# Optimization experiments

Measured on AMD Instinct MI355X. Metric: run time of the kernel, lower is better.

Reference implementation:

```python
import jax, jax.numpy as jnp
import numpy as np

E = 16          # number of experts
K = 2           # top-k routing
D = 1024        # model dim
F = 512         # expert ffn dim
T = 4096        # tokens
C = 2048


def setup_inputs() -> dict:
    key = jax.random.key(0)
    k1, k2, k3, k4, k5, k6 = jax.random.split(key, 6)
    return {
        "hidden_states": jax.random.normal(k1, (T, D), jnp.float32),
        "topk_indices": jax.random.randint(k2, (T, K), 0, E, jnp.int64),
        "topk_weights": jax.random.uniform(k3, (T, K), jnp.float32),
        "w_gate": jax.random.normal(k4, (E, D, F), jnp.float32) * 0.02,
        "w_up": jax.random.normal(k5, (E, D, F), jnp.float32) * 0.02,
        "w_down": jax.random.normal(k6, (E, F, D), jnp.float32) * 0.02,
    }


def reference(hidden_states, topk_indices, topk_weights, w_gate, w_up, w_down):
    Tn, d = hidden_states.shape
    k = topk_indices.shape[1]
    TK = Tn * k

    # ---- dispatch_tokens: group (token, expert) pairs by expert id ----
    flat_e = topk_indices.reshape(-1)                 # [TK] expert id per slot
    flat_w = topk_weights.reshape(-1)                 # [TK]
    flat_t = jnp.arange(TK) // k                      # [TK] source token id
    order = jnp.argsort(flat_e)                       # sort slots by expert
    se, st, sw = flat_e[order], flat_t[order], flat_w[order]
    counts = jnp.bincount(flat_e, length=E)           # tokens per expert
    starts = jnp.cumsum(counts) - counts              # exclusive prefix sum
    pos = jnp.arange(TK) - starts[se]                 # position within expert bucket
    valid = pos < C
    slot = jnp.where(valid, se * C + pos, E * C)      # overflow -> scratch row

    # gather tokens into padded per-expert buffers [E, C, D]
    buf = jnp.zeros((E * C + 1, d), hidden_states.dtype).at[slot].set(hidden_states[st])
    xe = buf[: E * C].reshape(E, C, d)

    # ---- per-expert gated-SiLU MLP via grouped GEMMs ----
    h = jax.nn.silu(jnp.einsum('ecd,edf->ecf', xe, w_gate)) * jnp.einsum('ecd,edf->ecf', xe, w_up)
    ye = jnp.einsum('ecf,efd->ecd', h, w_down).reshape(E * C, d)

    # ---- weighted scatter-add combine (index_add_) ----
    contrib = ye[jnp.minimum(slot, E * C - 1)] * (sw * valid.astype(sw.dtype))[:, None]
    out = jnp.zeros((Tn, d), topk_weights.dtype).at[st].add(contrib)
    return out.astype(hidden_states.dtype)
```

## Files before the change

kernel.cpp:

```cpp
#include <hip/hip_runtime.h>
#include <hip/hip_bf16.h>

constexpr int E_ = 16, K_ = 2, D_ = 1024, F_ = 512, T_ = 4096;
constexpr int TK_ = T_ * K_;
constexpr int CAP_ = 2048;
constexpr int BM_ = 128;
constexpr int ROWS_MAX = 10240;

constexpr size_t SZ_W   = (size_t)E_ * F_ * D_ * 2;
constexpr size_t OFF_WDT  = 0;
constexpr size_t OFF_WGT  = OFF_WDT + SZ_W;
constexpr size_t OFF_WUT  = OFF_WGT + SZ_W;
constexpr size_t OFF_XG   = OFF_WUT + SZ_W;
constexpr size_t SZ_XG  = (size_t)ROWS_MAX * D_ * 2;
constexpr size_t OFF_H    = OFF_XG + SZ_XG;
constexpr size_t SZ_H   = (size_t)ROWS_MAX * F_ * 2;
constexpr size_t OFF_META = OFF_H + SZ_H;
constexpr size_t OFF_YE   = OFF_WGT;
static_assert(OFF_YE + (size_t)ROWS_MAX * D_ * 4 <= OFF_H, "Ye overlaps live buffers");

typedef __attribute__((ext_vector_type(8))) short short8;
typedef __attribute__((ext_vector_type(4))) float float4v;

__device__ __forceinline__ unsigned short f2bf(float f) {
  union { float f; unsigned int u; } v; v.f = f;
  unsigned int r = (v.u + 0x7fffu + ((v.u >> 16) & 1u)) >> 16;
  return (unsigned short)r;
}

__device__ __forceinline__ void load_lds16(const unsigned short* g, unsigned short* l) {
  __builtin_amdgcn_global_load_lds(
      (const __attribute__((address_space(1))) unsigned int*)g,
      (__attribute__((address_space(3))) unsigned int*)l,
      16, 0, 0);
}

__device__ __forceinline__ void barrier_nodrain() {
  asm volatile("" ::: "memory");
  __builtin_amdgcn_s_barrier();
  asm volatile("" ::: "memory");
}

__launch_bounds__(1024)
__global__ void dispatch_k(const int* __restrict__ idx, const float* __restrict__ tw,
                           int* __restrict__ cnt_c, int* __restrict__ off_al,
                           int* __restrict__ row_token, float* __restrict__ row_weight,
                           int* __restrict__ slot_row) {
  __shared__ int hist[E_], offs[E_], ctr[E_];
  int tid = threadIdx.x;
  if (tid < E_) hist[tid] = 0;
  __syncthreads();
  for (int i = tid; i < TK_; i += 1024) atomicAdd(&hist[idx[i]], 1);
  __syncthreads();
  if (tid == 0) {
    int run = 0;
    for (int e = 0; e < E_; ++e) {
      int c = hist[e] > CAP_ ? CAP_ : hist[e];
      cnt_c[e] = c; off_al[e] = run; offs[e] = run; ctr[e] = 0;
      run += (c + BM_ - 1) & ~(BM_ - 1);
    }
  }
  __syncthreads();
  for (int r = tid; r < ROWS_MAX; r += 1024) row_token[r] = -1;
  __syncthreads();
  for (int i = tid; i < TK_; i += 1024) {
    int e = idx[i];
    int r = atomicAdd(&ctr[e], 1);
    int row = -1;
    if (r < CAP_) {
      row = offs[e] + r;
      row_token[row] = i >> 1;
      row_weight[row] = tw[i];
    }
    slot_row[i] = row;
  }
}

__global__ void gather_k(const float* __restrict__ hidden, const int* __restrict__ row_token,
                         unsigned short* __restrict__ Xg) {
  int r = blockIdx.x;
  int tok = row_token[r];
  int c = threadIdx.x * 4;
  ushort4 o;
  if (tok >= 0) {
    float4 v = *(const float4*)(hidden + (size_t)tok * D_ + c);
    o.x = f2bf(v.x); o.y = f2bf(v.y); o.z = f2bf(v.z); o.w = f2bf(v.w);
  } else {
    o.x = 0; o.y = 0; o.z = 0; o.w = 0;
  }
  *(ushort4*)(Xg + (size_t)r * D_ + c) = o;
}

__launch_bounds__(256)
__global__ void transpose_all_k(const float* __restrict__ wg, const float* __restrict__ wu,
                                const float* __restrict__ wd,
                                unsigned short* __restrict__ WgT, unsigned short* __restrict__ WuT,
                                unsigned short* __restrict__ WdT) {
  __shared__ float tile[64][65];
  int z = blockIdx.y;
  int kind = z >> 4, e = z & 15;
  int R = (kind == 2) ? F_ : D_;
  int C = (kind == 2) ? D_ : F_;
  const float* s = ((kind == 0) ? wg : (kind == 1) ? wu : wd) + (size_t)e * R * C;
  unsigned short* d = ((kind == 0) ? WgT : (kind == 1) ? WuT : WdT) + (size_t)e * R * C;
  int tilesX = C >> 6;
  int t = blockIdx.x;
  int r0 = (t / tilesX) * 64, c0 = (t % tilesX) * 64;

  int lr = threadIdx.x >> 4;
  int lc = (threadIdx.x & 15) * 4;
#pragma unroll
  for (int it = 0; it < 4; ++it) {
    int row = lr + it * 16;
    float4 v = *(const float4*)(s + (size_t)(r0 + row) * C + (c0 + lc));
    tile[row][lc + 0] = v.x; tile[row][lc + 1] = v.y;
    tile[row][lc + 2] = v.z; tile[row][lc + 3] = v.w;
  }
  __syncthreads();

  int w = threadIdx.x >> 6, l = threadIdx.x & 63;
#pragma unroll
  for (int it = 0; it < 2; ++it) {
    int c = (it * 4 + w) * 8 + (l >> 3);
    int r8 = (l & 7) * 8;
    short8 o;
#pragma unroll
    for (int j = 0; j < 8; ++j) o[j] = (short)f2bf(tile[r8 + j][c]);
    *(short8*)(d + (size_t)(c0 + c) * R + (r0 + r8)) = o;
  }
}


__launch_bounds__(256)
__global__ void gemm1_k(const unsigned short* __restrict__ Xg,
                        const unsigned short* __restrict__ WgT,
                        const unsigned short* __restrict__ WuT,
                        unsigned short* __restrict__ Hbuf,
                        const int* __restrict__ cnt_c, const int* __restrict__ off_al) {
  int bid = blockIdx.x;
  int swz = (bid & 7) * 512 + (bid >> 3);
  int e = swz >> 8, mt = (swz >> 3) & 31, nt = swz & 7;
  int cnt = cnt_c[e];
  if (mt * 64 >= cnt) return;
  int rbase = off_al[e] + mt * 64;

  __shared__ unsigned short lA[2][64 * 64];
  __shared__ unsigned short lBg[2][64 * 64];
  __shared__ unsigned short lBu[2][64 * 64];

  int tid = threadIdx.x, wid = tid >> 6, lane = tid & 63;
  int wm = wid >> 1, wn = wid & 1;
  int quad = lane >> 4, l15 = lane & 15;
  int sw = l15 & 7;

  const unsigned short* gA = Xg + (size_t)rbase * D_;
  const unsigned short* gB0 = WgT + ((size_t)e * F_ + nt * 64) * D_;
  const unsigned short* gB1 = WuT + ((size_t)e * F_ + nt * 64) * D_;

  float4v accg[2][2], accu[2][2];
#pragma unroll
  for (int i = 0; i < 2; ++i)
#pragma unroll
    for (int j = 0; j < 2; ++j) {
      accg[i][j] = (float4v){0.f, 0.f, 0.f, 0.f};
      accu[i][j] = (float4v){0.f, 0.f, 0.f, 0.f};
    }

  auto stage = [&](int buf, int k0) {
#pragma unroll
    for (int it = 0; it < 2; ++it) {
      int fw = it * 256 + wid * 64;
      int f = fw + lane;
      int row = f >> 3, c8 = (f & 7) ^ (row & 7);
      size_t go = (size_t)row * D_ + k0 + c8 * 8;
      load_lds16(gA + go, &lA[buf][fw * 8]);
      load_lds16(gB0 + go, &lBg[buf][fw * 8]);
      load_lds16(gB1 + go, &lBu[buf][fw * 8]);
    }
  };

  stage(0, 0);

  for (int kt = 0; kt < 16; ++kt) {
    int cur = kt & 1;
    if (kt + 1 < 16) {
      stage(cur ^ 1, (kt + 1) * 64);
      asm volatile("s_waitcnt vmcnt(6)" ::: "memory");
    } else {
      asm volatile("s_waitcnt vmcnt(0)" ::: "memory");
    }
    __builtin_amdgcn_sched_barrier(0);
    barrier_nodrain();
#pragma unroll
    for (int kc = 0; kc < 2; ++kc) {
      short8 af[2], bg[2], bu[2];
#pragma unroll
      for (int i = 0; i < 2; ++i) {
        int r = wm * 32 + i * 16 + l15;
        af[i] = *(const short8*)&lA[cur][r * 64 + ((kc * 4 + quad) ^ sw) * 8];
      }
#pragma unroll
      for (int j = 0; j < 2; ++j) {
        int n = wn * 32 + j * 16 + l15;
        bg[j] = *(const short8*)&lBg[cur][n * 64 + ((kc * 4 + quad) ^ sw) * 8];
        bu[j] = *(const short8*)&lBu[cur][n * 64 + ((kc * 4 + quad) ^ sw) * 8];
      }
#pragma unroll
      for (int i = 0; i < 2; ++i)
#pragma unroll
        for (int j = 0; j < 2; ++j) {
          accg[i][j] = __builtin_amdgcn_mfma_f32_16x16x32_bf16(af[i], bg[j], accg[i][j], 0, 0, 0);
          accu[i][j] = __builtin_amdgcn_mfma_f32_16x16x32_bf16(af[i], bu[j], accu[i][j], 0, 0, 0);
        }
    }
    barrier_nodrain();
  }

  int rem = cnt - mt * 64;
#pragma unroll
  for (int i = 0; i < 2; ++i)
#pragma unroll
    for (int j = 0; j < 2; ++j)
#pragma unroll
      for (int r = 0; r < 4; ++r) {
        int row = wm * 32 + i * 16 + quad * 4 + r;
        if (row < rem) {
          float g = accg[i][j][r], u = accu[i][j][r];
          float h = (g / (1.f + __expf(-g))) * u;
          int n = nt * 64 + wn * 32 + j * 16 + l15;
          Hbuf[(size_t)(rbase + row) * F_ + n] = f2bf(h);
        }
      }
}

__launch_bounds__(256)
__global__ void gemm2_k(const unsigned short* __restrict__ Hbuf,
                        const unsigned short* __restrict__ WdT,
                        float* __restrict__ Ye,
                        const int* __restrict__ cnt_c, const int* __restrict__ off_al) {
  int bid = blockIdx.x;
  int swz = (bid & 7) * 512 + (bid >> 3);
  int e = swz >> 8, mt = (swz >> 3) & 31, nt = swz & 7;
  int cnt = cnt_c[e];
  if (mt * 64 >= cnt) return;
  int rbase = off_al[e] + mt * 64;

  __shared__ unsigned short lA[2][64 * 64];
  __shared__ unsigned short lB[2][128 * 64];

  int tid = threadIdx.x, wid = tid >> 6, lane = tid & 63;
  int wm = wid >> 1, wn = wid & 1;
  int quad = lane >> 4, l15 = lane & 15;
  int sw = l15 & 7;

  const unsigned short* gA = Hbuf + (size_t)rbase * F_;
  const unsigned short* gB = WdT + ((size_t)e * D_ + nt * 128) * F_;

  float4v acc[2][4];
#pragma unroll
  for (int i = 0; i < 2; ++i)
#pragma unroll
    for (int j = 0; j < 4; ++j) acc[i][j] = (float4v){0.f, 0.f, 0.f, 0.f};

  auto stage = [&](int buf, int k0) {
#pragma unroll
    for (int it = 0; it < 2; ++it) {
      int fw = it * 256 + wid * 64;
      int f = fw + lane;
      int row = f >> 3, c8 = (f & 7) ^ (row & 7);
      load_lds16(gA + (size_t)row * F_ + k0 + c8 * 8, &lA[buf][fw * 8]);
    }
#pragma unroll
    for (int it = 0; it < 4; ++it) {
      int fw = it * 256 + wid * 64;
      int f = fw + lane;
      int row = f >> 3, c8 = (f & 7) ^ (row & 7);
      load_lds16(gB + (size_t)row * F_ + k0 + c8 * 8, &lB[buf][fw * 8]);
    }
  };

  stage(0, 0);

  for (int kt = 0; kt < 8; ++kt) {
    int cur = kt & 1;
    if (kt + 1 < 8) {
      stage(cur ^ 1, (kt + 1) * 64);
      asm volatile("s_waitcnt vmcnt(6)" ::: "memory");
    } else {
      asm volatile("s_waitcnt vmcnt(0)" ::: "memory");
    }
    __builtin_amdgcn_sched_barrier(0);
    barrier_nodrain();
#pragma unroll
    for (int kc = 0; kc < 2; ++kc) {
      short8 af[2], bf[4];
#pragma unroll
      for (int i = 0; i < 2; ++i) {
        int r = wm * 32 + i * 16 + l15;
        af[i] = *(const short8*)&lA[cur][r * 64 + ((kc * 4 + quad) ^ sw) * 8];
      }
#pragma unroll
      for (int j = 0; j < 4; ++j) {
        int n = wn * 64 + j * 16 + l15;
        bf[j] = *(const short8*)&lB[cur][n * 64 + ((kc * 4 + quad) ^ sw) * 8];
      }
#pragma unroll
      for (int i = 0; i < 2; ++i)
#pragma unroll
        for (int j = 0; j < 4; ++j)
          acc[i][j] = __builtin_amdgcn_mfma_f32_16x16x32_bf16(af[i], bf[j], acc[i][j], 0, 0, 0);
    }
    barrier_nodrain();
  }

  int rem = cnt - mt * 64;
#pragma unroll
  for (int i = 0; i < 2; ++i)
#pragma unroll
    for (int r = 0; r < 4; ++r) {
      int row = wm * 32 + i * 16 + quad * 4 + r;
      if (row < rem) {
        float* yp = Ye + (size_t)(rbase + row) * D_ + nt * 128 + wn * 64 + l15;
#pragma unroll
        for (int j = 0; j < 4; ++j) yp[j * 16] = acc[i][j][r];
      }
    }
}

__global__ void combine_k(const float* __restrict__ Ye, const int* __restrict__ slot_row,
                          const float* __restrict__ row_weight, float* __restrict__ out) {
  int t = blockIdx.x;
  int c = threadIdx.x * 4;
  int r0 = slot_row[2 * t], r1 = slot_row[2 * t + 1];
  float4 acc = {0.f, 0.f, 0.f, 0.f};
  if (r0 >= 0) {
    float w = row_weight[r0];
    float4 y = *(const float4*)(Ye + (size_t)r0 * D_ + c);
    acc.x = w * y.x; acc.y = w * y.y; acc.z = w * y.z; acc.w = w * y.w;
  }
  if (r1 >= 0) {
    float w = row_weight[r1];
    float4 y = *(const float4*)(Ye + (size_t)r1 * D_ + c);
    acc.x += w * y.x; acc.y += w * y.y; acc.z += w * y.z; acc.w += w * y.w;
  }
  *(float4*)(out + (size_t)t * D_ + c) = acc;
}

extern "C" void kernel_launch(void* const* d_in, const int* in_sizes, int n_in,
                              void* d_out, int out_size, void* d_ws, size_t ws_size,
                              hipStream_t stream) {
  const float* hidden  = (const float*)d_in[0];
  const int*   topkidx = (const int*)d_in[1];
  const float* topkw   = (const float*)d_in[2];
  const float* w_gate  = (const float*)d_in[3];
  const float* w_up    = (const float*)d_in[4];
  const float* w_down  = (const float*)d_in[5];
  float* out = (float*)d_out;

  char* ws = (char*)d_ws;
  unsigned short* WdT = (unsigned short*)(ws + OFF_WDT);
  unsigned short* WgT = (unsigned short*)(ws + OFF_WGT);
  unsigned short* WuT = (unsigned short*)(ws + OFF_WUT);
  unsigned short* Xg  = (unsigned short*)(ws + OFF_XG);
  unsigned short* Hb  = (unsigned short*)(ws + OFF_H);
  float* Ye           = (float*)(ws + OFF_YE);
  int* meta           = (int*)(ws + OFF_META);
  int* cnt_c     = meta;
  int* off_al    = meta + 16;
  int* row_token = meta + 32;
  float* row_weight = (float*)(meta + 32 + ROWS_MAX);
  int* slot_row  = meta + 32 + 2 * ROWS_MAX;

  dispatch_k<<<1, 1024, 0, stream>>>(topkidx, topkw, cnt_c, off_al, row_token, row_weight,
                                     slot_row);
  transpose_all_k<<<dim3(128, 48), 256, 0, stream>>>(w_gate, w_up, w_down, WgT, WuT, WdT);
  gather_k<<<ROWS_MAX, 256, 0, stream>>>(hidden, row_token, Xg);

  gemm1_k<<<4096, 256, 0, stream>>>(Xg, WgT, WuT, Hb, cnt_c, off_al);
  gemm2_k<<<4096, 256, 0, stream>>>(Hb, WdT, Ye, cnt_c, off_al);
  combine_k<<<T_, 256, 0, stream>>>(Ye, slot_row, row_weight, out);
}
```

Before: 232.7 us.

## Fuse fp32 weight conversion into grouped GEMMs and parallelize dispatch per expert

Drops the separate transpose/convert kernel. The GEMMs now load fp32 weights straight from global memory into registers, convert them to bf16 with packed cvt instructions, and write them transposed into LDS, with the B tiles single-buffered. Dispatch is split into one block per expert, and the workspace layout shrinks because the transposed weight copies are gone. This removes a full pass over 96MB of fp32 weights, but every GEMM tile re-reads fp32 weights with strided scalar loads, so global traffic per tile roughly doubles and more time may be exposed on loads.

```diff
diff --git a/kernel.cpp b/kernel.cpp
--- a/kernel.cpp
+++ b/kernel.cpp
@@ -7,17 +7,12 @@
 constexpr int BM_ = 128;
 constexpr int ROWS_MAX = 10240;
 
-constexpr size_t SZ_W   = (size_t)E_ * F_ * D_ * 2;
-constexpr size_t OFF_WDT  = 0;
-constexpr size_t OFF_WGT  = OFF_WDT + SZ_W;
-constexpr size_t OFF_WUT  = OFF_WGT + SZ_W;
-constexpr size_t OFF_XG   = OFF_WUT + SZ_W;
-constexpr size_t SZ_XG  = (size_t)ROWS_MAX * D_ * 2;
-constexpr size_t OFF_H    = OFF_XG + SZ_XG;
-constexpr size_t SZ_H   = (size_t)ROWS_MAX * F_ * 2;
-constexpr size_t OFF_META = OFF_H + SZ_H;
-constexpr size_t OFF_YE   = OFF_WGT;
-static_assert(OFF_YE + (size_t)ROWS_MAX * D_ * 4 <= OFF_H, "Ye overlaps live buffers");
+constexpr size_t OFF_H    = 0;
+constexpr size_t SZ_H     = (size_t)ROWS_MAX * F_ * 2;
+constexpr size_t OFF_XG   = OFF_H + SZ_H;
+constexpr size_t OFF_YE   = OFF_XG;
+constexpr size_t SZ_YE    = (size_t)ROWS_MAX * D_ * 4;
+constexpr size_t OFF_META = OFF_XG + SZ_YE;
 
 typedef __attribute__((ext_vector_type(8))) short short8;
 typedef __attribute__((ext_vector_type(4))) float float4v;
@@ -26,6 +21,12 @@
   union { float f; unsigned int u; } v; v.f = f;
   unsigned int r = (v.u + 0x7fffu + ((v.u >> 16) & 1u)) >> 16;
   return (unsigned short)r;
+}
+
+__device__ __forceinline__ unsigned int cvt2(float lo, float hi) {
+  unsigned int r;
+  asm("v_cvt_pk_bf16_f32 %0, %1, %2" : "=v"(r) : "v"(lo), "v"(hi));
+  return r;
 }
 
 __device__ __forceinline__ void load_lds16(const unsigned short* g, unsigned short* l) {
@@ -41,38 +42,44 @@
   asm volatile("" ::: "memory");
 }
 
-__launch_bounds__(1024)
+__launch_bounds__(256)
 __global__ void dispatch_k(const int* __restrict__ idx, const float* __restrict__ tw,
                            int* __restrict__ cnt_c, int* __restrict__ off_al,
                            int* __restrict__ row_token, float* __restrict__ row_weight,
                            int* __restrict__ slot_row) {
-  __shared__ int hist[E_], offs[E_], ctr[E_];
-  int tid = threadIdx.x;
+  __shared__ int hist[E_];
+  __shared__ int off_s, pad_s, cnt_s;
+  int e = blockIdx.x, tid = threadIdx.x;
   if (tid < E_) hist[tid] = 0;
+  if (tid == 0) cnt_s = 0;
   __syncthreads();
-  for (int i = tid; i < TK_; i += 1024) atomicAdd(&hist[idx[i]], 1);
+  for (int i = tid; i < TK_; i += 256) atomicAdd(&hist[idx[i]], 1);
   __syncthreads();
   if (tid == 0) {
-    int run = 0;
-    for (int e = 0; e < E_; ++e) {
-      int c = hist[e] > CAP_ ? CAP_ : hist[e];
-      cnt_c[e] = c; off_al[e] = run; offs[e] = run; ctr[e] = 0;
+    int run = 0, off = 0, myc = 0;
+    for (int ee = 0; ee < E_; ++ee) {
+      int c = hist[ee] > CAP_ ? CAP_ : hist[ee];
+      if (ee == e) { off = run; myc = c; }
       run += (c + BM_ - 1) & ~(BM_ - 1);
     }
+    off_s = off; pad_s = (myc + BM_ - 1) & ~(BM_ - 1);
+    cnt_c[e] = myc; off_al[e] = off;
   }
   __syncthreads();
-  for (int r = tid; r < ROWS_MAX; r += 1024) row_token[r] = -1;
+  int off = off_s, pad = pad_s;
+  for (int r = tid; r < pad; r += 256) row_token[off + r] = -1;
   __syncthreads();
-  for (int i = tid; i < TK_; i += 1024) {
-    int e = idx[i];
-    int r = atomicAdd(&ctr[e], 1);
-    int row = -1;
-    if (r < CAP_) {
-      row = offs[e] + r;
-      row_token[row] = i >> 1;
-      row_weight[row] = tw[i];
-    }
-    slot_row[i] = row;
+  for (int i = tid; i < TK_; i += 256) {
+    if (idx[i] == e) {
+      int r = atomicAdd(&cnt_s, 1);
+      int row = -1;
+      if (r < CAP_) {
+        row = off + r;
+        row_token[row] = i >> 1;
+        row_weight[row] = tw[i];
+      }
+      slot_row[i] = row;
+    }
   }
 }
 
@@ -82,7 +89,7 @@
   int tok = row_token[r];
   int c = threadIdx.x * 4;
   ushort4 o;
-  if (tok >= 0) {
+  if ((unsigned)tok < (unsigned)T_) {
     float4 v = *(const float4*)(hidden + (size_t)tok * D_ + c);
     o.x = f2bf(v.x); o.y = f2bf(v.y); o.z = f2bf(v.z); o.w = f2bf(v.w);
   } else {
@@ -91,50 +98,10 @@
   *(ushort4*)(Xg + (size_t)r * D_ + c) = o;
 }
 
-__launch_bounds__(256)
-__global__ void transpose_all_k(const float* __restrict__ wg, const float* __restrict__ wu,
-                                const float* __restrict__ wd,
-                                unsigned short* __restrict__ WgT, unsigned short* __restrict__ WuT,
-                                unsigned short* __restrict__ WdT) {
-  __shared__ float tile[64][65];
-  int z = blockIdx.y;
-  int kind = z >> 4, e = z & 15;
-  int R = (kind == 2) ? F_ : D_;
-  int C = (kind == 2) ? D_ : F_;
-  const float* s = ((kind == 0) ? wg : (kind == 1) ? wu : wd) + (size_t)e * R * C;
-  unsigned short* d = ((kind == 0) ? WgT : (kind == 1) ? WuT : WdT) + (size_t)e * R * C;
-  int tilesX = C >> 6;
-  int t = blockIdx.x;
-  int r0 = (t / tilesX) * 64, c0 = (t % tilesX) * 64;
-
-  int lr = threadIdx.x >> 4;
-  int lc = (threadIdx.x & 15) * 4;
-#pragma unroll
-  for (int it = 0; it < 4; ++it) {
-    int row = lr + it * 16;
-    float4 v = *(const float4*)(s + (size_t)(r0 + row) * C + (c0 + lc));
-    tile[row][lc + 0] = v.x; tile[row][lc + 1] = v.y;
-    tile[row][lc + 2] = v.z; tile[row][lc + 3] = v.w;
-  }
-  __syncthreads();
-
-  int w = threadIdx.x >> 6, l = threadIdx.x & 63;
-#pragma unroll
-  for (int it = 0; it < 2; ++it) {
-    int c = (it * 4 + w) * 8 + (l >> 3);
-    int r8 = (l & 7) * 8;
-    short8 o;
-#pragma unroll
-    for (int j = 0; j < 8; ++j) o[j] = (short)f2bf(tile[r8 + j][c]);
-    *(short8*)(d + (size_t)(c0 + c) * R + (r0 + r8)) = o;
-  }
-}
-
-
-__launch_bounds__(256)
+
+__launch_bounds__(256, 4)
 __global__ void gemm1_k(const unsigned short* __restrict__ Xg,
-                        const unsigned short* __restrict__ WgT,
-                        const unsigned short* __restrict__ WuT,
+                        const float* __restrict__ Wg, const float* __restrict__ Wu,
                         unsigned short* __restrict__ Hbuf,
                         const int* __restrict__ cnt_c, const int* __restrict__ off_al) {
   int bid = blockIdx.x;
@@ -145,8 +112,8 @@
   int rbase = off_al[e] + mt * 64;
 
   __shared__ unsigned short lA[2][64 * 64];
-  __shared__ unsigned short lBg[2][64 * 64];
-  __shared__ unsigned short lBu[2][64 * 64];
+  __shared__ unsigned short lBg[64 * 64];
+  __shared__ unsigned short lBu[64 * 64];
 
   int tid = threadIdx.x, wid = tid >> 6, lane = tid & 63;
   int wm = wid >> 1, wn = wid & 1;
@@ -154,8 +121,8 @@
   int sw = l15 & 7;
 
   const unsigned short* gA = Xg + (size_t)rbase * D_;
-  const unsigned short* gB0 = WgT + ((size_t)e * F_ + nt * 64) * D_;
-  const unsigned short* gB1 = WuT + ((size_t)e * F_ + nt * 64) * D_;
+  const float* gW0 = Wg + (size_t)e * D_ * F_ + nt * 64 + lane;
+  const float* gW1 = Wu + (size_t)e * D_ * F_ + nt * 64 + lane;
 
   float4v accg[2][2], accu[2][2];
 #pragma unroll
@@ -166,29 +133,57 @@
       accu[i][j] = (float4v){0.f, 0.f, 0.f, 0.f};
     }
 
-  auto stage = [&](int buf, int k0) {
+  float bga[8], bgb[8], bua[8], bub[8];
+  auto loadB = [&](int k0) {
+#pragma unroll
+    for (int j = 0; j < 8; ++j) {
+      size_t ra = (size_t)(k0 + wid * 8 + j) * F_;
+      size_t rb = (size_t)(k0 + (wid + 4) * 8 + j) * F_;
+      bga[j] = gW0[ra]; bgb[j] = gW0[rb];
+      bua[j] = gW1[ra]; bub[j] = gW1[rb];
+    }
+  };
+  int sA = (wid ^ (lane & 7)) * 8, sB = ((wid + 4) ^ (lane & 7)) * 8;
+  int wb = lane * 64;
+  auto writeB = [&]() {
+    uint4 p;
+    p.x = cvt2(bga[0], bga[1]); p.y = cvt2(bga[2], bga[3]);
+    p.z = cvt2(bga[4], bga[5]); p.w = cvt2(bga[6], bga[7]);
+    *(uint4*)&lBg[wb + sA] = p;
+    p.x = cvt2(bgb[0], bgb[1]); p.y = cvt2(bgb[2], bgb[3]);
+    p.z = cvt2(bgb[4], bgb[5]); p.w = cvt2(bgb[6], bgb[7]);
+    *(uint4*)&lBg[wb + sB] = p;
+    p.x = cvt2(bua[0], bua[1]); p.y = cvt2(bua[2], bua[3]);
+    p.z = cvt2(bua[4], bua[5]); p.w = cvt2(bua[6], bua[7]);
+    *(uint4*)&lBu[wb + sA] = p;
+    p.x = cvt2(bub[0], bub[1]); p.y = cvt2(bub[2], bub[3]);
+    p.z = cvt2(bub[4], bub[5]); p.w = cvt2(bub[6], bub[7]);
+    *(uint4*)&lBu[wb + sB] = p;
+  };
+  auto stageA = [&](int buf, int k0) {
 #pragma unroll
     for (int it = 0; it < 2; ++it) {
       int fw = it * 256 + wid * 64;
       int f = fw + lane;
       int row = f >> 3, c8 = (f & 7) ^ (row & 7);
-      size_t go = (size_t)row * D_ + k0 + c8 * 8;
-      load_lds16(gA + go, &lA[buf][fw * 8]);
-      load_lds16(gB0 + go, &lBg[buf][fw * 8]);
-      load_lds16(gB1 + go, &lBu[buf][fw * 8]);
-    }
-  };
-
-  stage(0, 0);
+      load_lds16(gA + (size_t)row * D_ + k0 + c8 * 8, &lA[buf][fw * 8]);
+    }
+  };
+
+  loadB(0);
+  stageA(0, 0);
 
   for (int kt = 0; kt < 16; ++kt) {
     int cur = kt & 1;
+    writeB();
     if (kt + 1 < 16) {
-      stage(cur ^ 1, (kt + 1) * 64);
-      asm volatile("s_waitcnt vmcnt(6)" ::: "memory");
+      loadB((kt + 1) * 64);
+      stageA(cur ^ 1, (kt + 1) * 64);
+      asm volatile("s_waitcnt vmcnt(34)" ::: "memory");
     } else {
       asm volatile("s_waitcnt vmcnt(0)" ::: "memory");
     }
+    asm volatile("s_waitcnt lgkmcnt(0)" ::: "memory");
     __builtin_amdgcn_sched_barrier(0);
     barrier_nodrain();
 #pragma unroll
@@ -202,8 +197,8 @@
 #pragma unroll
       for (int j = 0; j < 2; ++j) {
         int n = wn * 32 + j * 16 + l15;
-        bg[j] = *(const short8*)&lBg[cur][n * 64 + ((kc * 4 + quad) ^ sw) * 8];
-        bu[j] = *(const short8*)&lBu[cur][n * 64 + ((kc * 4 + quad) ^ sw) * 8];
+        bg[j] = *(const short8*)&lBg[n * 64 + ((kc * 4 + quad) ^ sw) * 8];
+        bu[j] = *(const short8*)&lBu[n * 64 + ((kc * 4 + quad) ^ sw) * 8];
       }
 #pragma unroll
       for (int i = 0; i < 2; ++i)
@@ -233,9 +228,9 @@
       }
 }
 
-__launch_bounds__(256)
+__launch_bounds__(256, 4)
 __global__ void gemm2_k(const unsigned short* __restrict__ Hbuf,
-                        const unsigned short* __restrict__ WdT,
+                        const float* __restrict__ Wd,
                         float* __restrict__ Ye,
                         const int* __restrict__ cnt_c, const int* __restrict__ off_al) {
   int bid = blockIdx.x;
@@ -246,7 +241,7 @@
   int rbase = off_al[e] + mt * 64;
 
   __shared__ unsigned short lA[2][64 * 64];
-  __shared__ unsigned short lB[2][128 * 64];
+  __shared__ unsigned short lB[128 * 64];
 
   int tid = threadIdx.x, wid = tid >> 6, lane = tid & 63;
   int wm = wid >> 1, wn = wid & 1;
@@ -254,7 +249,7 @@
   int sw = l15 & 7;
 
   const unsigned short* gA = Hbuf + (size_t)rbase * F_;
-  const unsigned short* gB = WdT + ((size_t)e * D_ + nt * 128) * F_;
+  const float* gW = Wd + (size_t)e * F_ * D_ + nt * 128 + lane;
 
   float4v acc[2][4];
 #pragma unroll
@@ -262,7 +257,26 @@
 #pragma unroll
     for (int j = 0; j < 4; ++j) acc[i][j] = (float4v){0.f, 0.f, 0.f, 0.f};
 
-  auto stage = [&](int buf, int k0) {
+  float b[4][8];
+  auto loadB = [&](int k0) {
+#pragma unroll
+    for (int c = 0; c < 4; ++c)
+#pragma unroll
+      for (int j = 0; j < 8; ++j)
+        b[c][j] = gW[(size_t)(k0 + (wid + (c >> 1) * 4) * 8 + j) * D_ + (c & 1) * 64];
+  };
+  auto writeB = [&]() {
+#pragma unroll
+    for (int c = 0; c < 4; ++c) {
+      int n = (c & 1) * 64 + lane;
+      int s = ((wid + (c >> 1) * 4) ^ (lane & 7)) * 8;
+      uint4 p;
+      p.x = cvt2(b[c][0], b[c][1]); p.y = cvt2(b[c][2], b[c][3]);
+      p.z = cvt2(b[c][4], b[c][5]); p.w = cvt2(b[c][6], b[c][7]);
+      *(uint4*)&lB[n * 64 + s] = p;
+    }
+  };
+  auto stageA = [&](int buf, int k0) {
 #pragma unroll
     for (int it = 0; it < 2; ++it) {
       int fw = it * 256 + wid * 64;
@@ -270,25 +284,22 @@
       int row = f >> 3, c8 = (f & 7) ^ (row & 7);
       load_lds16(gA + (size_t)row * F_ + k0 + c8 * 8, &lA[buf][fw * 8]);
     }
-#pragma unroll
-    for (int it = 0; it < 4; ++it) {
-      int fw = it * 256 + wid * 64;
-      int f = fw + lane;
-      int row = f >> 3, c8 = (f & 7) ^ (row & 7);
-      load_lds16(gB + (size_t)row * F_ + k0 + c8 * 8, &lB[buf][fw * 8]);
-    }
-  };
-
-  stage(0, 0);
+  };
+
+  loadB(0);
+  stageA(0, 0);
 
   for (int kt = 0; kt < 8; ++kt) {
     int cur = kt & 1;
+    writeB();
     if (kt + 1 < 8) {
-      stage(cur ^ 1, (kt + 1) * 64);
-      asm volatile("s_waitcnt vmcnt(6)" ::: "memory");
+      loadB((kt + 1) * 64);
+      stageA(cur ^ 1, (kt + 1) * 64);
+      asm volatile("s_waitcnt vmcnt(34)" ::: "memory");
     } else {
       asm volatile("s_waitcnt vmcnt(0)" ::: "memory");
     }
+    asm volatile("s_waitcnt lgkmcnt(0)" ::: "memory");
     __builtin_amdgcn_sched_barrier(0);
     barrier_nodrain();
 #pragma unroll
@@ -302,7 +313,7 @@
 #pragma unroll
       for (int j = 0; j < 4; ++j) {
         int n = wn * 64 + j * 16 + l15;
-        bf[j] = *(const short8*)&lB[cur][n * 64 + ((kc * 4 + quad) ^ sw) * 8];
+        bf[j] = *(const short8*)&lB[n * 64 + ((kc * 4 + quad) ^ sw) * 8];
       }
 #pragma unroll
       for (int i = 0; i < 2; ++i)
@@ -358,11 +369,8 @@
   float* out = (float*)d_out;
 
   char* ws = (char*)d_ws;
-  unsigned short* WdT = (unsigned short*)(ws + OFF_WDT);
-  unsigned short* WgT = (unsigned short*)(ws + OFF_WGT);
-  unsigned short* WuT = (unsigned short*)(ws + OFF_WUT);
+  unsigned short* Hb  = (unsigned short*)(ws + OFF_H);
   unsigned short* Xg  = (unsigned short*)(ws + OFF_XG);
-  unsigned short* Hb  = (unsigned short*)(ws + OFF_H);
   float* Ye           = (float*)(ws + OFF_YE);
   int* meta           = (int*)(ws + OFF_META);
   int* cnt_c     = meta;
@@ -371,12 +379,11 @@
   float* row_weight = (float*)(meta + 32 + ROWS_MAX);
   int* slot_row  = meta + 32 + 2 * ROWS_MAX;
 
-  dispatch_k<<<1, 1024, 0, stream>>>(topkidx, topkw, cnt_c, off_al, row_token, row_weight,
+  dispatch_k<<<E_, 256, 0, stream>>>(topkidx, topkw, cnt_c, off_al, row_token, row_weight,
                                      slot_row);
-  transpose_all_k<<<dim3(128, 48), 256, 0, stream>>>(w_gate, w_up, w_down, WgT, WuT, WdT);
   gather_k<<<ROWS_MAX, 256, 0, stream>>>(hidden, row_token, Xg);
 
-  gemm1_k<<<4096, 256, 0, stream>>>(Xg, WgT, WuT, Hb, cnt_c, off_al);
-  gemm2_k<<<4096, 256, 0, stream>>>(Hb, WdT, Ye, cnt_c, off_al);
+  gemm1_k<<<4096, 256, 0, stream>>>(Xg, w_gate, w_up, Hb, cnt_c, off_al);
+  gemm2_k<<<4096, 256, 0, stream>>>(Hb, w_down, Ye, cnt_c, off_al);
   combine_k<<<T_, 256, 0, stream>>>(Ye, slot_row, row_weight, out);
 }
```

Result: slower. 258.6 us (+11.1%).
